# Performance work log

Hardware: AMD Instinct MI355X
Metric: run time of the kernel (lower is better)

The kernel has to match this reference:

```python
import jax, jax.numpy as jnp
import numpy as np

NB, NG = 131072, 32768            # n_bus, n_gen nodes
EBB, EGB, EBG = 2097152, 65536, 65536  # bus-bus, gen->bus, bus->gen edges
CIN, C, COUT = 32, 64, 32         # in_channels, n_channels, out_channels
NL, NT = 2, 5                     # n_layers, n_taps+1
EPS = 1e-5


def setup_inputs() -> dict:
    key = jax.random.key(0)
    ks = iter(jax.random.split(key, 40))
    rn = lambda shape, s=1.0: jax.random.normal(next(ks), shape, dtype=jnp.float32) * s
    ri = lambda shape, hi: jax.random.randint(next(ks), shape, 0, hi, dtype=jnp.int32)
    inp = {
        'x_bus': rn((NB, CIN)), 'x_gen': rn((NG, CIN)),
        'readin_W_bus': rn((CIN, C), CIN ** -0.5), 'readin_b_bus': jnp.zeros((C,), jnp.float32),
        'readin_W_gen': rn((CIN, C), CIN ** -0.5), 'readin_b_gen': jnp.zeros((C,), jnp.float32),
        'bn_gamma_bus': jnp.ones((NL, C), jnp.float32), 'bn_beta_bus': jnp.zeros((NL, C), jnp.float32),
        'bn_gamma_gen': jnp.ones((NL, C), jnp.float32), 'bn_beta_gen': jnp.zeros((NL, C), jnp.float32),
        'taps_W_bus': rn((NL, NT, C, C), C ** -0.5), 'taps_b_bus': jnp.zeros((NL, NT, C), jnp.float32),
        'taps_W_gen': rn((NL, NT, C, C), C ** -0.5), 'taps_b_gen': jnp.zeros((NL, NT, C), jnp.float32),
        'readout_W_bus': rn((C, COUT), C ** -0.5), 'readout_b_bus': jnp.zeros((COUT,), jnp.float32),
        'readout_W_gen': rn((C, COUT), C ** -0.5), 'readout_b_gen': jnp.zeros((COUT,), jnp.float32),
        'edge_bb': ri((2, EBB), NB),
        'edge_gb_src': ri((EGB,), NG), 'edge_gb_dst': ri((EGB,), NB),
        'edge_bg_src': ri((EBG,), NB), 'edge_bg_dst': ri((EBG,), NG),
    }
    return inp


def _lrelu(v):
    return jnp.where(v >= 0, v, 0.01 * v)  # nn.LeakyReLU default slope


def _bn(v, g, b):
    # training-mode BatchNorm over the node dimension (biased variance)
    m = jnp.mean(v, axis=0)
    s = jnp.var(v, axis=0)
    return (v - m) * jax.lax.rsqrt(s + EPS) * g + b


def reference(x_bus, x_gen,
              readin_W_bus, readin_b_bus, readin_W_gen, readin_b_gen,
              bn_gamma_bus, bn_beta_bus, bn_gamma_gen, bn_beta_gen,
              taps_W_bus, taps_b_bus, taps_W_gen, taps_b_gen,
              readout_W_bus, readout_b_bus, readout_W_gen, readout_b_gen,
              edge_bb, edge_gb_src, edge_gb_dst, edge_bg_src, edge_bg_dst):
    seg = jax.ops.segment_sum
    bbs, bbd = edge_bb[0], edge_bb[1]
    # readin (single HeteroDictLinear, plain_last)
    xb = x_bus @ readin_W_bus + readin_b_bus   # [NB, C]
    xg = x_gen @ readin_W_gen + readin_b_gen   # [NG, C]
    for l in range(NL):  # residual blocks: norm -> act -> (dropout p=0) -> graph filter -> +x
        yb = _lrelu(_bn(xb, bn_gamma_bus[l], bn_beta_bus[l]))
        yg = _lrelu(_bn(xg, bn_gamma_gen[l], bn_beta_gen[l]))
        zb = yb @ taps_W_bus[l, 0] + taps_b_bus[l, 0]
        zg = yg @ taps_W_gen[l, 0] + taps_b_gen[l, 0]
        cb, cg = yb, yg
        for k in range(1, NT):  # graph shift (scatter-add over hetero edges) + per-type tap
            nb = seg(cb[bbs], bbd, num_segments=NB) + seg(cg[edge_gb_src], edge_gb_dst, num_segments=NB)
            ng = seg(cb[edge_bg_src], edge_bg_dst, num_segments=NG)
            cb, cg = nb, ng
            zb = zb + cb @ taps_W_bus[l, k] + taps_b_bus[l, k]
            zg = zg + cg @ taps_W_gen[l, k] + taps_b_gen[l, k]
        xb = xb + zb
        xg = xg + zg
    out_b = xb @ readout_W_bus + readout_b_bus  # [NB, COUT]
    out_g = xg @ readout_W_gen + readout_b_gen  # [NG, COUT]
    return (out_b, out_g)
```

## Files before the change

### kernel.cpp

```cpp
#include <hip/hip_runtime.h>

#define NBUS 131072
#define NGEN 32768
#define NALL (NBUS + NGEN)
#define NEBB 2097152
#define NEGB 65536
#define NEBG 65536
#define NTILE (NALL / 64)
#define NTILE_BUS (NBUS / 64)
#define NGB 2560
#define CAPB 56
#define CAPG 24

typedef float f32x2 __attribute__((ext_vector_type(2)));
typedef float f32x4 __attribute__((ext_vector_type(4)));
typedef short s16x8 __attribute__((ext_vector_type(8)));
typedef unsigned short u16;

__device__ inline f32x2 bf2x2(unsigned v) {
  f32x2 r;
  r.x = __builtin_bit_cast(float, v << 16);
  r.y = __builtin_bit_cast(float, v & 0xFFFF0000u);
  return r;
}
__device__ inline u16 f2bf(float f) {
  unsigned u = __builtin_bit_cast(unsigned, f);
  unsigned r = u + 0x7FFFu + ((u >> 16) & 1u);
  return (u16)(r >> 16);
}
__device__ inline unsigned pack2bf(float a, float b) {
  return (unsigned)f2bf(a) | ((unsigned)f2bf(b) << 16);
}

__global__ void __launch_bounds__(256) k_convw(const float* __restrict__ tWb,
                                               const float* __restrict__ tWg,
                                               const float* __restrict__ roWb,
                                               const float* __restrict__ roWg,
                                               const float* __restrict__ riWb,
                                               const float* __restrict__ riWg,
                                               u16* __restrict__ wt,
                                               u16* __restrict__ rot,
                                               u16* __restrict__ riwt) {
  int t = blockIdx.x * 256 + threadIdx.x;
  int S = gridDim.x * 256;
  for (int i = t; i < 20 * 4096; i += S) {
    int mat = i >> 12, off = i & 4095, n = off >> 6, k = off & 63;
    const float* src = (mat < 10) ? tWb : tWg;
    int tap = (mat < 10) ? mat : mat - 10;
    wt[i] = f2bf(src[(size_t)tap * 4096 + k * 64 + n]);
  }
  for (int i = t; i < 2 * 2048; i += S) {
    int type = i >> 11, off = i & 2047, n = off >> 6, k = off & 63;
    const float* src = type ? roWg : roWb;
    rot[i] = f2bf(src[k * 32 + n]);
  }
  for (int i = t; i < 2 * 2048; i += S) {
    int type = i >> 11, off = i & 2047, n = off >> 5, k = off & 31;
    const float* src = type ? riWg : riWb;
    riwt[i] = f2bf(src[k * 64 + n]);
  }
}

__device__ inline void dev_fill(int bid, const int* __restrict__ bbSrc,
                                const int* __restrict__ bbDst,
                                const int* __restrict__ gbSrc,
                                const int* __restrict__ gbDst,
                                const int* __restrict__ bgSrc,
                                const int* __restrict__ bgDst,
                                int* __restrict__ busCnt, int* __restrict__ bgCnt,
                                int* __restrict__ busBkt, int* __restrict__ bgBkt) {
  const int g = bid & 7;
  const int tid = threadIdx.x;
  if (bid < 2048) {
    const int blk = bid >> 3;
    const int S = 256 * 256;
    int i = blk * 256 + tid;
    for (; i + 3 * S < NEBB; i += 4 * S) {
      int d0 = bbDst[i], d1 = bbDst[i + S], d2 = bbDst[i + 2 * S], d3 = bbDst[i + 3 * S];
      if ((d0 >> 14) == g) { int p = atomicAdd(&busCnt[d0], 1); busBkt[d0 * CAPB + p] = bbSrc[i]; }
      if ((d1 >> 14) == g) { int p = atomicAdd(&busCnt[d1], 1); busBkt[d1 * CAPB + p] = bbSrc[i + S]; }
      if ((d2 >> 14) == g) { int p = atomicAdd(&busCnt[d2], 1); busBkt[d2 * CAPB + p] = bbSrc[i + 2 * S]; }
      if ((d3 >> 14) == g) { int p = atomicAdd(&busCnt[d3], 1); busBkt[d3 * CAPB + p] = bbSrc[i + 3 * S]; }
    }
    for (; i < NEBB; i += S) {
      int d = bbDst[i];
      if ((d >> 14) == g) { int p = atomicAdd(&busCnt[d], 1); busBkt[d * CAPB + p] = bbSrc[i]; }
    }
  } else if (bid < 2304) {
    const int blk = (bid - 2048) >> 3;
    const int S = 32 * 256;
    for (int i = blk * 256 + tid; i < NEGB; i += S) {
      int d = gbDst[i];
      if ((d >> 14) == g) { int p = atomicAdd(&busCnt[d], 1); busBkt[d * CAPB + p] = gbSrc[i] + NBUS; }
    }
  } else {
    const int blk = (bid - 2304) >> 3;
    const int S = 32 * 256;
    for (int i = blk * 256 + tid; i < NEBG; i += S) {
      int d = bgDst[i];
      if ((d >> 12) == g) { int p = atomicAdd(&bgCnt[d], 1); bgBkt[d * CAPG + p] = bgSrc[i]; }
    }
  }
}

__device__ inline void dev_readin(int tile, const float* __restrict__ xbus,
                                  const float* __restrict__ xgen,
                                  const u16* __restrict__ riwt,
                                  const float* __restrict__ bb_,
                                  const float* __restrict__ bg_,
                                  float* __restrict__ y, float* __restrict__ stats) {
  __shared__ float sst[128];
  const bool isBus = tile < NTILE_BUS;
  const int tid = threadIdx.x, lane = tid & 63, wv = tid >> 6;
  const int m = lane & 15, kq = lane >> 4;
  const int grow = tile * 64 + wv * 16 + m;
  const float* xp = isBus ? &xbus[(size_t)grow * 32] : &xgen[(size_t)(grow - NBUS) * 32];
  s16x8 a;
#pragma unroll
  for (int j = 0; j < 8; j++) a[j] = (short)f2bf(xp[kq * 8 + j]);
  const u16* rb = riwt + (size_t)(isBus ? 0 : 1) * 2048;
  const float* bb = isBus ? bb_ : bg_;
  f32x4 acc[4];
#pragma unroll
  for (int cb = 0; cb < 4; cb++) {
    acc[cb] = (f32x4){0.f, 0.f, 0.f, 0.f};
    const u16* wp = rb + (cb * 16 + m) * 32 + kq * 8;
    s16x8 b = *(const s16x8*)wp;
    acc[cb] = __builtin_amdgcn_mfma_f32_16x16x32_bf16(a, b, acc[cb], 0, 0, 0);
  }
  if (tid < 128) sst[tid] = 0.f;
  __syncthreads();
  const int orow0 = tile * 64 + wv * 16 + kq * 4;
#pragma unroll
  for (int cb = 0; cb < 4; cb++) {
    int col = cb * 16 + m;
    float bv = bb[col];
    float s1 = 0.f, s2 = 0.f;
#pragma unroll
    for (int i = 0; i < 4; i++) {
      float yo = acc[cb][i] + bv;
      y[(size_t)(orow0 + i) * 64 + col] = yo;
      s1 += yo;
      s2 = fmaf(yo, yo, s2);
    }
    atomicAdd(&sst[col], s1);
    atomicAdd(&sst[64 + col], s2);
  }
  __syncthreads();
  if (tid < 64) {
    atomicAdd(&stats[(isBus ? 0 : 128) + tid], sst[tid]);
    atomicAdd(&stats[(isBus ? 0 : 128) + 64 + tid], sst[64 + tid]);
  }
}

__global__ void __launch_bounds__(256) k_fill_readin(
    const int* __restrict__ bbSrc, const int* __restrict__ bbDst,
    const int* __restrict__ gbSrc, const int* __restrict__ gbDst,
    const int* __restrict__ bgSrc, const int* __restrict__ bgDst,
    int* __restrict__ busCnt, int* __restrict__ bgCnt,
    int* __restrict__ busBkt, int* __restrict__ bgBkt,
    const float* __restrict__ xbus, const float* __restrict__ xgen,
    const u16* __restrict__ riwt, const float* __restrict__ bb_,
    const float* __restrict__ bg_, float* __restrict__ y, float* __restrict__ stats) {
  if (blockIdx.x < 2560)
    dev_fill(blockIdx.x, bbSrc, bbDst, gbSrc, gbDst, bgSrc, bgDst,
             busCnt, bgCnt, busBkt, bgBkt);
  else
    dev_readin(blockIdx.x - 2560, xbus, xgen, riwt, bb_, bg_, y, stats);
}

__global__ void __launch_bounds__(256) k_norm(
    float* __restrict__ x, u16* __restrict__ c0, const float* __restrict__ stats,
    const float* __restrict__ gammaB, const float* __restrict__ betaB,
    const float* __restrict__ gammaG, const float* __restrict__ betaG,
    const u16* __restrict__ wt, const float* __restrict__ tbb,
    const float* __restrict__ tbg, int tapIdx) {
  __shared__ u16 yt[64][72];
  const int tile = blockIdx.x;
  const bool isBus = tile < NTILE_BUS;
  const int tid = threadIdx.x, lane = tid & 63, wv = tid >> 6;
  int so = isBus ? 0 : 128;
  float invN = isBus ? (1.0f / NBUS) : (1.0f / NGEN);
  float mn = stats[so + lane] * invN;
  float m2 = stats[so + 64 + lane] * invN;
  float rs = rsqrtf(m2 - mn * mn + 1e-5f);
  float scale = (isBus ? gammaB : gammaG)[lane] * rs;
  float shift = (isBus ? betaB : betaG)[lane] - mn * scale;
  unsigned* cu = (unsigned*)c0;
  int rw0 = tile * 64 + wv * 16;
  for (int i = 0; i < 16; i++) {
    int row = rw0 + i;
    float xv = x[(size_t)row * 64 + lane];
    float y = fmaf(xv, scale, shift);
    y = (y >= 0.f) ? y : 0.01f * y;
    float ypair = __shfl(y, lane ^ 1, 64);
    if ((lane & 1) == 0) {
      unsigned pk = pack2bf(y, ypair);
      cu[(size_t)row * 32 + (lane >> 1)] = pk;
      *(unsigned*)&yt[wv * 16 + i][lane] = pk;
    }
  }
  __syncthreads();
  const int m = lane & 15, kq = lane >> 4;
  const u16* wrow = wt + (size_t)((isBus ? 0 : 10) + tapIdx) * 4096;
  const float* bbase = isBus ? tbb : tbg;
  int lr = wv * 16 + m;
  s16x8 a0 = *(const s16x8*)&yt[lr][kq * 8];
  s16x8 a1 = *(const s16x8*)&yt[lr][32 + kq * 8];
  f32x4 acc[4];
#pragma unroll
  for (int cb = 0; cb < 4; cb++) acc[cb] = (f32x4){0.f, 0.f, 0.f, 0.f};
#pragma unroll
  for (int cb = 0; cb < 4; cb++) {
    const u16* wp = wrow + (cb * 16 + m) * 64 + kq * 8;
    s16x8 b0 = *(const s16x8*)&wp[0];
    s16x8 b1 = *(const s16x8*)&wp[32];
    acc[cb] = __builtin_amdgcn_mfma_f32_16x16x32_bf16(a0, b0, acc[cb], 0, 0, 0);
    acc[cb] = __builtin_amdgcn_mfma_f32_16x16x32_bf16(a1, b1, acc[cb], 0, 0, 0);
  }
  const int orow0 = tile * 64 + wv * 16 + kq * 4;
#pragma unroll
  for (int cb = 0; cb < 4; cb++) {
    int col = cb * 16 + m;
    float bsv = bbase[(size_t)tapIdx * 64 + col];
#pragma unroll
    for (int i = 0; i < 4; i++) {
      size_t idx = (size_t)(orow0 + i) * 64 + col;
      x[idx] += acc[cb][i] + bsv;
    }
  }
}

__device__ inline void dev_gather(int bid, const int* __restrict__ busBkt,
                                  const int* __restrict__ busCnt,
                                  const int* __restrict__ bgBkt,
                                  const int* __restrict__ bgCnt,
                                  const u16* __restrict__ src, u16* __restrict__ dst) {
  const int lane = threadIdx.x & 63;
  const int wv = threadIdx.x >> 6;
  const int grp = lane >> 3;
  const int sub = lane & 7;
  const int gb = grp << 3;
  const unsigned* s32 = (const unsigned*)src;
  unsigned* d32 = (unsigned*)dst;
  int rowBase = (bid * 4 + wv) * 8;
  for (int row0 = rowBase; row0 < NALL; row0 += NGB * 32) {
    int row = row0 + grp;
    int beg, end;
    const int* srt;
    if (row < NBUS) {
      beg = row * CAPB;
      end = beg + busCnt[row];
      srt = busBkt;
    } else {
      int rr = row - NBUS;
      beg = rr * CAPG;
      end = beg + bgCnt[rr];
      srt = bgBkt;
    }
    f32x2 a0 = {0.f, 0.f}, a1 = {0.f, 0.f}, a2 = {0.f, 0.f}, a3 = {0.f, 0.f};
    int last = end - 1;
    for (int e = beg; e < end; e += 8) {
      int ei = e + sub;
      int sv = srt[ei <= last ? ei : last];
      uint4 v[8];
#pragma unroll
      for (int j = 0; j < 8; j++) {
        int s = __shfl(sv, gb + j, 64);
        uint4 vv = *(const uint4*)&s32[(size_t)s * 32 + sub * 4];
        if (e + j > last) { vv.x = 0; vv.y = 0; vv.z = 0; vv.w = 0; }
        v[j] = vv;
      }
#pragma unroll
      for (int j = 0; j < 8; j++) {
        a0 += bf2x2(v[j].x);
        a1 += bf2x2(v[j].y);
        a2 += bf2x2(v[j].z);
        a3 += bf2x2(v[j].w);
      }
    }
    uint4 o;
    o.x = pack2bf(a0.x, a0.y);
    o.y = pack2bf(a1.x, a1.y);
    o.z = pack2bf(a2.x, a2.y);
    o.w = pack2bf(a3.x, a3.y);
    *(uint4*)&d32[(size_t)row * 32 + sub * 4] = o;
  }
}

__global__ void __launch_bounds__(256) k_gather(const int* __restrict__ busBkt,
                                                const int* __restrict__ busCnt,
                                                const int* __restrict__ bgBkt,
                                                const int* __restrict__ bgCnt,
                                                const u16* __restrict__ src,
                                                u16* __restrict__ dst) {
  dev_gather(blockIdx.x, busBkt, busCnt, bgBkt, bgCnt, src, dst);
}

__device__ inline void dev_tap2(int tile, const u16* __restrict__ cA,
                                const u16* __restrict__ cB, float* __restrict__ x,
                                const u16* __restrict__ wt,
                                const float* __restrict__ tbb,
                                const float* __restrict__ tbg,
                                int idxA, int idxB, float* __restrict__ stats) {
  __shared__ float sst[128];
  const bool isBus = tile < NTILE_BUS;
  const int row0 = tile * 64;
  const int tid = threadIdx.x, lane = tid & 63, wv = tid >> 6;
  const int m = lane & 15, kq = lane >> 4;
  const int arow = row0 + wv * 16 + m;
  const float* bbase = isBus ? tbb : tbg;
  const u16* wbase = wt + (size_t)(isBus ? 0 : 10) * 4096;
  f32x4 acc[4];
#pragma unroll
  for (int cb = 0; cb < 4; cb++) acc[cb] = (f32x4){0.f, 0.f, 0.f, 0.f};
  const u16* cs[2] = {cA, cB};
  const int idxs[2] = {idxA, idxB};
#pragma unroll
  for (int s = 0; s < 2; s++) {
    const u16* c = cs[s];
    s16x8 a0 = *(const s16x8*)&c[(size_t)arow * 64 + kq * 8];
    s16x8 a1 = *(const s16x8*)&c[(size_t)arow * 64 + 32 + kq * 8];
    const u16* wrow = wbase + (size_t)idxs[s] * 4096;
#pragma unroll
    for (int cb = 0; cb < 4; cb++) {
      const u16* wp = wrow + (cb * 16 + m) * 64 + kq * 8;
      s16x8 b0 = *(const s16x8*)&wp[0];
      s16x8 b1 = *(const s16x8*)&wp[32];
      acc[cb] = __builtin_amdgcn_mfma_f32_16x16x32_bf16(a0, b0, acc[cb], 0, 0, 0);
      acc[cb] = __builtin_amdgcn_mfma_f32_16x16x32_bf16(a1, b1, acc[cb], 0, 0, 0);
    }
  }
  if (stats) {
    if (tid < 128) sst[tid] = 0.f;
    __syncthreads();
  }
  const int orow0 = row0 + wv * 16 + kq * 4;
#pragma unroll
  for (int cb = 0; cb < 4; cb++) {
    int col = cb * 16 + m;
    float bsv = bbase[(size_t)idxA * 64 + col] + bbase[(size_t)idxB * 64 + col];
    float s1 = 0.f, s2 = 0.f;
#pragma unroll
    for (int i = 0; i < 4; i++) {
      size_t idx = (size_t)(orow0 + i) * 64 + col;
      float xo = x[idx] + acc[cb][i] + bsv;
      x[idx] = xo;
      s1 += xo;
      s2 = fmaf(xo, xo, s2);
    }
    if (stats) {
      atomicAdd(&sst[col], s1);
      atomicAdd(&sst[64 + col], s2);
    }
  }
  if (stats) {
    __syncthreads();
    if (tid < 64) {
      atomicAdd(&stats[(isBus ? 0 : 128) + tid], sst[tid]);
      atomicAdd(&stats[(isBus ? 0 : 128) + 64 + tid], sst[64 + tid]);
    }
  }
}

__global__ void __launch_bounds__(256) k_tap2(const u16* __restrict__ cA,
                                              const u16* __restrict__ cB,
                                              float* __restrict__ x,
                                              const u16* __restrict__ wt,
                                              const float* __restrict__ tbb,
                                              const float* __restrict__ tbg,
                                              int idxA, int idxB,
                                              float* __restrict__ stats) {
  dev_tap2(blockIdx.x, cA, cB, x, wt, tbb, tbg, idxA, idxB, stats);
}

__global__ void __launch_bounds__(256) k_gather_tap2(
    const int* __restrict__ busBkt, const int* __restrict__ busCnt,
    const int* __restrict__ bgBkt, const int* __restrict__ bgCnt,
    const u16* __restrict__ gsrc, u16* __restrict__ gdst,
    const u16* __restrict__ cA, const u16* __restrict__ cB, float* __restrict__ x,
    const u16* __restrict__ wt, const float* __restrict__ tbb,
    const float* __restrict__ tbg, int idxA, int idxB) {
  if (blockIdx.x < NGB)
    dev_gather(blockIdx.x, busBkt, busCnt, bgBkt, bgCnt, gsrc, gdst);
  else
    dev_tap2(blockIdx.x - NGB, cA, cB, x, wt, tbb, tbg, idxA, idxB, (float*)nullptr);
}

__global__ void __launch_bounds__(256) k_tap2_ro(
    const u16* __restrict__ cA, const u16* __restrict__ cB,
    const float* __restrict__ x, const u16* __restrict__ wt,
    const float* __restrict__ tbb, const float* __restrict__ tbg,
    int idxA, int idxB, const u16* __restrict__ rot,
    const float* __restrict__ robb, const float* __restrict__ robg,
    float* __restrict__ out) {
  __shared__ u16 yt[64][72];
  const int tile = blockIdx.x;
  const bool isBus = tile < NTILE_BUS;
  const int row0 = tile * 64;
  const int tid = threadIdx.x, lane = tid & 63, wv = tid >> 6;
  const int m = lane & 15, kq = lane >> 4;
  const int arow = row0 + wv * 16 + m;
  const float* bbase = isBus ? tbb : tbg;
  const u16* wbase = wt + (size_t)(isBus ? 0 : 10) * 4096;
  f32x4 acc[4];
#pragma unroll
  for (int cb = 0; cb < 4; cb++) acc[cb] = (f32x4){0.f, 0.f, 0.f, 0.f};
  const u16* cs[2] = {cA, cB};
  const int idxs[2] = {idxA, idxB};
#pragma unroll
  for (int s = 0; s < 2; s++) {
    const u16* c = cs[s];
    s16x8 a0 = *(const s16x8*)&c[(size_t)arow * 64 + kq * 8];
    s16x8 a1 = *(const s16x8*)&c[(size_t)arow * 64 + 32 + kq * 8];
    const u16* wrow = wbase + (size_t)idxs[s] * 4096;
#pragma unroll
    for (int cb = 0; cb < 4; cb++) {
      const u16* wp = wrow + (cb * 16 + m) * 64 + kq * 8;
      s16x8 b0 = *(const s16x8*)&wp[0];
      s16x8 b1 = *(const s16x8*)&wp[32];
      acc[cb] = __builtin_amdgcn_mfma_f32_16x16x32_bf16(a0, b0, acc[cb], 0, 0, 0);
      acc[cb] = __builtin_amdgcn_mfma_f32_16x16x32_bf16(a1, b1, acc[cb], 0, 0, 0);
    }
  }
  const int lrow0 = wv * 16 + kq * 4;
#pragma unroll
  for (int cb = 0; cb < 4; cb++) {
    int col = cb * 16 + m;
    float bsv = bbase[(size_t)idxA * 64 + col] + bbase[(size_t)idxB * 64 + col];
#pragma unroll
    for (int i = 0; i < 4; i++) {
      float xo = x[(size_t)(row0 + lrow0 + i) * 64 + col] + acc[cb][i] + bsv;
      yt[lrow0 + i][col] = f2bf(xo);
    }
  }
  __syncthreads();
  int lr = wv * 16 + m;
  s16x8 a0 = *(const s16x8*)&yt[lr][kq * 8];
  s16x8 a1 = *(const s16x8*)&yt[lr][32 + kq * 8];
  const u16* rbase = rot + (size_t)(isBus ? 0 : 1) * 2048;
  f32x4 racc[2];
  racc[0] = (f32x4){0.f, 0.f, 0.f, 0.f};
  racc[1] = (f32x4){0.f, 0.f, 0.f, 0.f};
#pragma unroll
  for (int cb = 0; cb < 2; cb++) {
    const u16* wp = rbase + (cb * 16 + m) * 64 + kq * 8;
    s16x8 b0 = *(const s16x8*)&wp[0];
    s16x8 b1 = *(const s16x8*)&wp[32];
    racc[cb] = __builtin_amdgcn_mfma_f32_16x16x32_bf16(a0, b0, racc[cb], 0, 0, 0);
    racc[cb] = __builtin_amdgcn_mfma_f32_16x16x32_bf16(a1, b1, racc[cb], 0, 0, 0);
  }
  const float* bb = isBus ? robb : robg;
  const int orow0 = row0 + wv * 16 + kq * 4;
#pragma unroll
  for (int cb = 0; cb < 2; cb++) {
    int col = cb * 16 + m;
    float bv = bb[col];
#pragma unroll
    for (int i = 0; i < 4; i++)
      out[(size_t)(orow0 + i) * 32 + col] = racc[cb][i] + bv;
  }
}

extern "C" void kernel_launch(void* const* d_in, const int* in_sizes, int n_in,
                              void* d_out, int out_size, void* d_ws, size_t ws_size,
                              hipStream_t stream) {
  const float* x_bus = (const float*)d_in[0];
  const float* x_gen = (const float*)d_in[1];
  const float* riWb = (const float*)d_in[2];
  const float* ribb = (const float*)d_in[3];
  const float* riWg = (const float*)d_in[4];
  const float* ribg = (const float*)d_in[5];
  const float* bng_b = (const float*)d_in[6];
  const float* bnb_b = (const float*)d_in[7];
  const float* bng_g = (const float*)d_in[8];
  const float* bnb_g = (const float*)d_in[9];
  const float* tWb = (const float*)d_in[10];
  const float* tbb = (const float*)d_in[11];
  const float* tWg = (const float*)d_in[12];
  const float* tbg = (const float*)d_in[13];
  const float* roWb = (const float*)d_in[14];
  const float* robb = (const float*)d_in[15];
  const float* roWg = (const float*)d_in[16];
  const float* robg = (const float*)d_in[17];
  const int* ebb = (const int*)d_in[18];
  const int* gb_src = (const int*)d_in[19];
  const int* gb_dst = (const int*)d_in[20];
  const int* bg_src = (const int*)d_in[21];
  const int* bg_dst = (const int*)d_in[22];
  const int* bb_src = ebb;
  const int* bb_dst = ebb + NEBB;

  char* p = (char*)d_ws;
  auto take = [&](size_t bytes) -> void* {
    void* r = (void*)p;
    p += (bytes + 255) & ~(size_t)255;
    return r;
  };
  float* x = (float*)take((size_t)NALL * 64 * 4);
  u16* b0 = (u16*)take((size_t)NALL * 64 * 2);
  u16* b1 = (u16*)take((size_t)NALL * 64 * 2);
  u16* b2 = (u16*)take((size_t)NALL * 64 * 2);
  int* bus_bkt = (int*)take((size_t)NBUS * CAPB * 4);
  int* bg_bkt = (int*)take((size_t)NGEN * CAPG * 4);
  u16* wt = (u16*)take((size_t)20 * 4096 * 2);
  u16* rot = (u16*)take((size_t)2 * 2048 * 2);
  u16* riwt = (u16*)take((size_t)2 * 2048 * 2);
  int* bus_cnt = (int*)take((size_t)NBUS * 4);
  int* bg_cnt = (int*)take((size_t)NGEN * 4);
  float* stats0 = (float*)take(256 * 4);
  float* stats1 = (float*)take(256 * 4);
  size_t zlen = (char*)p - (char*)bus_cnt;
  if ((size_t)(p - (char*)d_ws) > ws_size) return;

  hipMemsetAsync(bus_cnt, 0, zlen, stream);
  k_convw<<<320, 256, 0, stream>>>(tWb, tWg, roWb, roWg, riWb, riWg, wt, rot, riwt);

  k_fill_readin<<<5120, 256, 0, stream>>>(bb_src, bb_dst, gb_src, gb_dst, bg_src, bg_dst,
                                          bus_cnt, bg_cnt, bus_bkt, bg_bkt,
                                          x_bus, x_gen, riwt, ribb, ribg, x, stats0);

  k_norm<<<NTILE, 256, 0, stream>>>(x, b0, stats0, bng_b, bnb_b, bng_g, bnb_g,
                                    wt, tbb, tbg, 0);
  k_gather<<<NGB, 256, 0, stream>>>(bus_bkt, bus_cnt, bg_bkt, bg_cnt, b0, b1);
  k_gather<<<NGB, 256, 0, stream>>>(bus_bkt, bus_cnt, bg_bkt, bg_cnt, b1, b2);
  k_gather_tap2<<<NGB + NTILE, 256, 0, stream>>>(bus_bkt, bus_cnt, bg_bkt, bg_cnt,
                                                 b2, b0, b1, b2, x, wt, tbb, tbg, 1, 2);
  k_gather<<<NGB, 256, 0, stream>>>(bus_bkt, bus_cnt, bg_bkt, bg_cnt, b0, b1);
  k_tap2<<<NTILE, 256, 0, stream>>>(b0, b1, x, wt, tbb, tbg, 3, 4, stats1);

  k_norm<<<NTILE, 256, 0, stream>>>(x, b0, stats1, bng_b + 64, bnb_b + 64,
                                    bng_g + 64, bnb_g + 64, wt, tbb, tbg, 5);
  k_gather<<<NGB, 256, 0, stream>>>(bus_bkt, bus_cnt, bg_bkt, bg_cnt, b0, b1);
  k_gather<<<NGB, 256, 0, stream>>>(bus_bkt, bus_cnt, bg_bkt, bg_cnt, b1, b2);
  k_gather_tap2<<<NGB + NTILE, 256, 0, stream>>>(bus_bkt, bus_cnt, bg_bkt, bg_cnt,
                                                 b2, b0, b1, b2, x, wt, tbb, tbg, 6, 7);
  k_gather<<<NGB, 256, 0, stream>>>(bus_bkt, bus_cnt, bg_bkt, bg_cnt, b0, b1);
  k_tap2_ro<<<NTILE, 256, 0, stream>>>(b0, b1, x, wt, tbb, tbg, 8, 9,
                                       rot, robb, robg, (float*)d_out);
}
```

Measured before the change: 741.6 us.

## Split bf16 feature buffers into 8 channel-slice planes for gather locality

The bf16 feature buffers move from row-major [N][64] to eight channel-group planes of [N][8] (16 bytes per row per plane). The gather kernel now assigns each block to a single plane, with 4 lanes per row each loading 4 bytes, so each plane's working set is smaller and more likely to stay in cache during random neighbor reads. The tap kernels stage the sliced layout into shared memory before running MFMA, which adds shared-memory traffic and a barrier. Gather loads shrink from 16 to 4 bytes per lane, which raises the number of memory instructions.

```diff
diff --git a/kernel.cpp b/kernel.cpp
--- a/kernel.cpp
+++ b/kernel.cpp
@@ -186,7 +186,9 @@
   float rs = rsqrtf(m2 - mn * mn + 1e-5f);
   float scale = (isBus ? gammaB : gammaG)[lane] * rs;
   float shift = (isBus ? betaB : betaG)[lane] - mn * scale;
-  unsigned* cu = (unsigned*)c0;
+  unsigned* slu = (unsigned*)c0;
+  const int sg = lane >> 3;
+  const int scc = (lane & 7) >> 1;
   int rw0 = tile * 64 + wv * 16;
   for (int i = 0; i < 16; i++) {
     int row = rw0 + i;
@@ -196,7 +198,7 @@
     float ypair = __shfl(y, lane ^ 1, 64);
     if ((lane & 1) == 0) {
       unsigned pk = pack2bf(y, ypair);
-      cu[(size_t)row * 32 + (lane >> 1)] = pk;
+      slu[((size_t)sg * NALL + row) * 4 + scc] = pk;
       *(unsigned*)&yt[wv * 16 + i][lane] = pk;
     }
   }
@@ -236,16 +238,18 @@
                                   const int* __restrict__ bgBkt,
                                   const int* __restrict__ bgCnt,
                                   const u16* __restrict__ src, u16* __restrict__ dst) {
+  const int g = bid & 7;
+  const int blk = bid >> 3;
   const int lane = threadIdx.x & 63;
   const int wv = threadIdx.x >> 6;
-  const int grp = lane >> 3;
-  const int sub = lane & 7;
-  const int gb = grp << 3;
-  const unsigned* s32 = (const unsigned*)src;
-  unsigned* d32 = (unsigned*)dst;
-  int rowBase = (bid * 4 + wv) * 8;
-  for (int row0 = rowBase; row0 < NALL; row0 += NGB * 32) {
-    int row = row0 + grp;
+  const int grp = lane >> 2;
+  const int cc = lane & 3;
+  const int gb = grp << 2;
+  const unsigned* s32 = (const unsigned*)src + (size_t)g * NALL * 4;
+  unsigned* d32 = (unsigned*)dst + (size_t)g * NALL * 4;
+  const int stride = (NGB >> 3) * 64;
+  for (int row0 = blk * 64; row0 < NALL; row0 += stride) {
+    int row = row0 + wv * 16 + grp;
     int beg, end;
     const int* srt;
     if (row < NBUS) {
@@ -261,30 +265,27 @@
     f32x2 a0 = {0.f, 0.f}, a1 = {0.f, 0.f}, a2 = {0.f, 0.f}, a3 = {0.f, 0.f};
     int last = end - 1;
     for (int e = beg; e < end; e += 8) {
-      int ei = e + sub;
-      int sv = srt[ei <= last ? ei : last];
-      uint4 v[8];
-#pragma unroll
-      for (int j = 0; j < 8; j++) {
-        int s = __shfl(sv, gb + j, 64);
-        uint4 vv = *(const uint4*)&s32[(size_t)s * 32 + sub * 4];
-        if (e + j > last) { vv.x = 0; vv.y = 0; vv.z = 0; vv.w = 0; }
-        v[j] = vv;
+      int ei0 = e + cc, ei1 = e + 4 + cc;
+      int sv0 = srt[ei0 <= last ? ei0 : last];
+      int sv1 = srt[ei1 <= last ? ei1 : last];
+      unsigned v[8];
+#pragma unroll
+      for (int j = 0; j < 4; j++) {
+        int s = __shfl(sv0, gb + j, 64);
+        unsigned vv = s32[(size_t)s * 4 + cc];
+        v[j] = (e + j > last) ? 0u : vv;
       }
 #pragma unroll
-      for (int j = 0; j < 8; j++) {
-        a0 += bf2x2(v[j].x);
-        a1 += bf2x2(v[j].y);
-        a2 += bf2x2(v[j].z);
-        a3 += bf2x2(v[j].w);
+      for (int j = 0; j < 4; j++) {
+        int s = __shfl(sv1, gb + j, 64);
+        unsigned vv = s32[(size_t)s * 4 + cc];
+        v[4 + j] = (e + 4 + j > last) ? 0u : vv;
       }
-    }
-    uint4 o;
-    o.x = pack2bf(a0.x, a0.y);
-    o.y = pack2bf(a1.x, a1.y);
-    o.z = pack2bf(a2.x, a2.y);
-    o.w = pack2bf(a3.x, a3.y);
-    *(uint4*)&d32[(size_t)row * 32 + sub * 4] = o;
+      a0 += bf2x2(v[0]); a1 += bf2x2(v[1]); a2 += bf2x2(v[2]); a3 += bf2x2(v[3]);
+      a0 += bf2x2(v[4]); a1 += bf2x2(v[5]); a2 += bf2x2(v[6]); a3 += bf2x2(v[7]);
+    }
+    f32x2 acc = (a0 + a1) + (a2 + a3);
+    d32[(size_t)row * 4 + cc] = pack2bf(acc.x, acc.y);
   }
 }
 
@@ -297,31 +298,45 @@
   dev_gather(blockIdx.x, busBkt, busCnt, bgBkt, bgCnt, src, dst);
 }
 
+__device__ inline void dev_stage(const u16* __restrict__ c, int row0,
+                                 u16 (*yt)[72]) {
+  const int tid = threadIdx.x;
+  const int r = tid >> 2, cc = tid & 3;
+  const unsigned* c32 = (const unsigned*)c;
+#pragma unroll
+  for (int g = 0; g < 8; g++) {
+    unsigned v = c32[((size_t)g * NALL + row0 + r) * 4 + cc];
+    *(unsigned*)&yt[r][g * 8 + cc * 2] = v;
+  }
+}
+
 __device__ inline void dev_tap2(int tile, const u16* __restrict__ cA,
                                 const u16* __restrict__ cB, float* __restrict__ x,
                                 const u16* __restrict__ wt,
                                 const float* __restrict__ tbb,
                                 const float* __restrict__ tbg,
                                 int idxA, int idxB, float* __restrict__ stats) {
+  __shared__ u16 ytA[64][72];
+  __shared__ u16 ytB[64][72];
   __shared__ float sst[128];
   const bool isBus = tile < NTILE_BUS;
   const int row0 = tile * 64;
   const int tid = threadIdx.x, lane = tid & 63, wv = tid >> 6;
   const int m = lane & 15, kq = lane >> 4;
-  const int arow = row0 + wv * 16 + m;
+  dev_stage(cA, row0, ytA);
+  dev_stage(cB, row0, ytB);
+  if (stats && tid < 128) sst[tid] = 0.f;
+  __syncthreads();
   const float* bbase = isBus ? tbb : tbg;
   const u16* wbase = wt + (size_t)(isBus ? 0 : 10) * 4096;
+  const int lr = wv * 16 + m;
   f32x4 acc[4];
 #pragma unroll
   for (int cb = 0; cb < 4; cb++) acc[cb] = (f32x4){0.f, 0.f, 0.f, 0.f};
-  const u16* cs[2] = {cA, cB};
-  const int idxs[2] = {idxA, idxB};
-#pragma unroll
-  for (int s = 0; s < 2; s++) {
-    const u16* c = cs[s];
-    s16x8 a0 = *(const s16x8*)&c[(size_t)arow * 64 + kq * 8];
-    s16x8 a1 = *(const s16x8*)&c[(size_t)arow * 64 + 32 + kq * 8];
-    const u16* wrow = wbase + (size_t)idxs[s] * 4096;
+  {
+    s16x8 a0 = *(const s16x8*)&ytA[lr][kq * 8];
+    s16x8 a1 = *(const s16x8*)&ytA[lr][32 + kq * 8];
+    const u16* wrow = wbase + (size_t)idxA * 4096;
 #pragma unroll
     for (int cb = 0; cb < 4; cb++) {
       const u16* wp = wrow + (cb * 16 + m) * 64 + kq * 8;
@@ -331,9 +346,18 @@
       acc[cb] = __builtin_amdgcn_mfma_f32_16x16x32_bf16(a1, b1, acc[cb], 0, 0, 0);
     }
   }
-  if (stats) {
-    if (tid < 128) sst[tid] = 0.f;
-    __syncthreads();
+  {
+    s16x8 a0 = *(const s16x8*)&ytB[lr][kq * 8];
+    s16x8 a1 = *(const s16x8*)&ytB[lr][32 + kq * 8];
+    const u16* wrow = wbase + (size_t)idxB * 4096;
+#pragma unroll
+    for (int cb = 0; cb < 4; cb++) {
+      const u16* wp = wrow + (cb * 16 + m) * 64 + kq * 8;
+      s16x8 b0 = *(const s16x8*)&wp[0];
+      s16x8 b1 = *(const s16x8*)&wp[32];
+      acc[cb] = __builtin_amdgcn_mfma_f32_16x16x32_bf16(a0, b0, acc[cb], 0, 0, 0);
+      acc[cb] = __builtin_amdgcn_mfma_f32_16x16x32_bf16(a1, b1, acc[cb], 0, 0, 0);
+    }
   }
   const int orow0 = row0 + wv * 16 + kq * 4;
 #pragma unroll
@@ -394,26 +418,26 @@
     int idxA, int idxB, const u16* __restrict__ rot,
     const float* __restrict__ robb, const float* __restrict__ robg,
     float* __restrict__ out) {
-  __shared__ u16 yt[64][72];
+  __shared__ u16 ytA[64][72];
+  __shared__ u16 ytB[64][72];
   const int tile = blockIdx.x;
   const bool isBus = tile < NTILE_BUS;
   const int row0 = tile * 64;
   const int tid = threadIdx.x, lane = tid & 63, wv = tid >> 6;
   const int m = lane & 15, kq = lane >> 4;
-  const int arow = row0 + wv * 16 + m;
+  dev_stage(cA, row0, ytA);
+  dev_stage(cB, row0, ytB);
+  __syncthreads();
   const float* bbase = isBus ? tbb : tbg;
   const u16* wbase = wt + (size_t)(isBus ? 0 : 10) * 4096;
+  const int lr = wv * 16 + m;
   f32x4 acc[4];
 #pragma unroll
   for (int cb = 0; cb < 4; cb++) acc[cb] = (f32x4){0.f, 0.f, 0.f, 0.f};
-  const u16* cs[2] = {cA, cB};
-  const int idxs[2] = {idxA, idxB};
-#pragma unroll
-  for (int s = 0; s < 2; s++) {
-    const u16* c = cs[s];
-    s16x8 a0 = *(const s16x8*)&c[(size_t)arow * 64 + kq * 8];
-    s16x8 a1 = *(const s16x8*)&c[(size_t)arow * 64 + 32 + kq * 8];
-    const u16* wrow = wbase + (size_t)idxs[s] * 4096;
+  {
+    s16x8 a0 = *(const s16x8*)&ytA[lr][kq * 8];
+    s16x8 a1 = *(const s16x8*)&ytA[lr][32 + kq * 8];
+    const u16* wrow = wbase + (size_t)idxA * 4096;
 #pragma unroll
     for (int cb = 0; cb < 4; cb++) {
       const u16* wp = wrow + (cb * 16 + m) * 64 + kq * 8;
@@ -423,6 +447,20 @@
       acc[cb] = __builtin_amdgcn_mfma_f32_16x16x32_bf16(a1, b1, acc[cb], 0, 0, 0);
     }
   }
+  {
+    s16x8 a0 = *(const s16x8*)&ytB[lr][kq * 8];
+    s16x8 a1 = *(const s16x8*)&ytB[lr][32 + kq * 8];
+    const u16* wrow = wbase + (size_t)idxB * 4096;
+#pragma unroll
+    for (int cb = 0; cb < 4; cb++) {
+      const u16* wp = wrow + (cb * 16 + m) * 64 + kq * 8;
+      s16x8 b0 = *(const s16x8*)&wp[0];
+      s16x8 b1 = *(const s16x8*)&wp[32];
+      acc[cb] = __builtin_amdgcn_mfma_f32_16x16x32_bf16(a0, b0, acc[cb], 0, 0, 0);
+      acc[cb] = __builtin_amdgcn_mfma_f32_16x16x32_bf16(a1, b1, acc[cb], 0, 0, 0);
+    }
+  }
+  __syncthreads();
   const int lrow0 = wv * 16 + kq * 4;
 #pragma unroll
   for (int cb = 0; cb < 4; cb++) {
@@ -431,13 +469,12 @@
 #pragma unroll
     for (int i = 0; i < 4; i++) {
       float xo = x[(size_t)(row0 + lrow0 + i) * 64 + col] + acc[cb][i] + bsv;
-      yt[lrow0 + i][col] = f2bf(xo);
-    }
-  }
-  __syncthreads();
-  int lr = wv * 16 + m;
-  s16x8 a0 = *(const s16x8*)&yt[lr][kq * 8];
-  s16x8 a1 = *(const s16x8*)&yt[lr][32 + kq * 8];
+      ytA[lrow0 + i][col] = f2bf(xo);
+    }
+  }
+  __syncthreads();
+  s16x8 a0 = *(const s16x8*)&ytA[lr][kq * 8];
+  s16x8 a1 = *(const s16x8*)&ytA[lr][32 + kq * 8];
   const u16* rbase = rot + (size_t)(isBus ? 0 : 1) * 2048;
   f32x4 racc[2];
   racc[0] = (f32x4){0.f, 0.f, 0.f, 0.f};
```

New measurement: 1.291 ms. 74.1% more time.
